# Kernel optimization log

Hardware: AMD Instinct MI355X
Metric: run time of the kernel (lower is better)

## Reference

```python
import jax, jax.numpy as jnp
import numpy as np

N = 100000
E = 3200000
F_IN = 128
HID = 16
C = 8


def setup_inputs() -> dict:
    key = jax.random.key(0)
    k1, k2, k3, k4 = jax.random.split(key, 4)
    x = jax.random.normal(k1, (N, F_IN), dtype=jnp.float32)
    edge_index = jax.random.randint(k2, (2, E), 0, N, dtype=jnp.int64)
    W1 = jax.random.normal(k3, (F_IN, HID), dtype=jnp.float32) * (1.0 / np.sqrt(F_IN))
    b1 = jnp.zeros((HID,), dtype=jnp.float32)
    W2 = jax.random.normal(k4, (HID, C), dtype=jnp.float32) * (1.0 / np.sqrt(HID))
    b2 = jnp.zeros((C,), dtype=jnp.float32)
    return {"x": x, "edge_index": edge_index, "W1": W1, "b1": b1, "W2": W2, "b2": b2, "num_nodes": N}


def gcn_conv(x, src, dst, norm, W, b, num_nodes):
    # x: [N, F_in], src/dst: [E+N] (self-loops appended), norm: [E+N]
    h = x @ W                                # dense transform first (small out dim)
    msg = h[src] * norm[:, None]             # gather + edgewise scale
    out = jax.ops.segment_sum(msg, dst, num_segments=num_nodes)  # scatter-add
    return out + b


def reference(x, edge_index, W1, b1, W2, b2, num_nodes):
    # GCN normalization with self-loops: D^-1/2 (A+I) D^-1/2
    loop = jnp.arange(num_nodes, dtype=edge_index.dtype)
    src = jnp.concatenate([edge_index[0], loop])
    dst = jnp.concatenate([edge_index[1], loop])
    deg = jax.ops.segment_sum(jnp.ones_like(dst, dtype=x.dtype), dst, num_segments=num_nodes)
    dinv = jnp.where(deg > 0, jax.lax.rsqrt(deg), 0.0)
    norm = dinv[src] * dinv[dst]             # [E+N]

    h = jax.nn.relu(gcn_conv(x, src, dst, norm, W1, b1, num_nodes))
    # Dropout(p=0.5) in eval mode -> identity
    logits = gcn_conv(h, src, dst, norm, W2, b2, num_nodes)
    return jax.nn.log_softmax(logits, axis=1)
```

## Files before the change

kernel.cpp:

```cpp
#include <hip/hip_runtime.h>
#include <hip/hip_fp16.h>
#include <math.h>

#define FIN 128
#define HID 16
#define NC 8
#define BSH 8
#define BUKN 256
#define MAXBUK 512
#define CAP 10240
#define EPT 8

__global__ void setup_kernel(const void* __restrict__ ei, int E, int N,
                             int* __restrict__ flag, int* __restrict__ pcur,
                             int nbuk) {
    int b = blockIdx.x * blockDim.x + threadIdx.x;
    if (b < nbuk) pcur[b * 16] = b * CAP;
    if (b == 0) {
        const long long* p = (const long long*)ei;
        int ok = 1;
        for (int i = 0; i < 16; ++i) {
            long long v = p[i];
            if (v < 0 || v >= (long long)N) { ok = 0; break; }
        }
        *flag = ok;
    }
}

__global__ __launch_bounds__(1024) void passA_kernel(
        const void* __restrict__ ei, int E, const int* __restrict__ flag,
        int* __restrict__ pcur, unsigned* __restrict__ pakbuf, int nbuk) {
    const int is64 = *flag;
    const int* __restrict__ e32 = (const int*)ei;
    const int vecOK = is64 ? ((E & 1) == 0) : ((E & 3) == 0);
    __shared__ int cnt[MAXBUK], sbase[MAXBUK];
    const int t = threadIdx.x;
    const int CH = 1024 * EPT;
    for (long long c0 = (long long)blockIdx.x * CH; c0 < E;
         c0 += (long long)gridDim.x * CH) {
        for (int i = t; i < nbuk; i += 1024) cnt[i] = 0;
        __syncthreads();
        const long long e0 = c0 + (long long)t * EPT;
        const bool full = vecOK && (e0 + EPT <= E);
        int bv[EPT], rk[EPT];
        unsigned pv[EPT];
        if (full) {
            int ds[EPT], ss[EPT];
            if (is64) {
                const int4* pd = (const int4*)(e32 + 2 * ((long long)E + e0));
                const int4* ps = (const int4*)(e32 + 2 * e0);
                int4 a = pd[0], b = pd[1], c = pd[2], d = pd[3];
                ds[0]=a.x; ds[1]=a.z; ds[2]=b.x; ds[3]=b.z;
                ds[4]=c.x; ds[5]=c.z; ds[6]=d.x; ds[7]=d.z;
                int4 e = ps[0], f = ps[1], g = ps[2], h = ps[3];
                ss[0]=e.x; ss[1]=e.z; ss[2]=f.x; ss[3]=f.z;
                ss[4]=g.x; ss[5]=g.z; ss[6]=h.x; ss[7]=h.z;
            } else {
                const int4* pd = (const int4*)(e32 + (long long)E + e0);
                const int4* ps = (const int4*)(e32 + e0);
                int4 a = pd[0], b = pd[1];
                ds[0]=a.x; ds[1]=a.y; ds[2]=a.z; ds[3]=a.w;
                ds[4]=b.x; ds[5]=b.y; ds[6]=b.z; ds[7]=b.w;
                int4 e = ps[0], f = ps[1];
                ss[0]=e.x; ss[1]=e.y; ss[2]=e.z; ss[3]=e.w;
                ss[4]=f.x; ss[5]=f.y; ss[6]=f.z; ss[7]=f.w;
            }
#pragma unroll
            for (int i = 0; i < EPT; ++i) {
                int dd = ds[i];
                bv[i] = dd >> BSH;
                pv[i] = (unsigned)ss[i] | ((unsigned)(dd & (BUKN - 1)) << 24);
                rk[i] = atomicAdd(&cnt[bv[i]], 1);
            }
        } else {
#pragma unroll
            for (int i = 0; i < EPT; ++i) {
                long long e = e0 + i;
                bv[i] = -1;
                if (e < E) {
                    int dd = e32[is64 ? 2 * ((long long)E + e) : ((long long)E + e)];
                    int ssc = e32[is64 ? 2 * e : e];
                    bv[i] = dd >> BSH;
                    pv[i] = (unsigned)ssc | ((unsigned)(dd & (BUKN - 1)) << 24);
                    rk[i] = atomicAdd(&cnt[bv[i]], 1);
                }
            }
        }
        __syncthreads();
        for (int i = t; i < nbuk; i += 1024)
            sbase[i] = cnt[i] ? atomicAdd(&pcur[i * 16], cnt[i]) : 0;
        __syncthreads();
#pragma unroll
        for (int i = 0; i < EPT; ++i) {
            if (bv[i] >= 0) {
                int pos = sbase[bv[i]] + rk[i];
                if (pos < (bv[i] + 1) * CAP) pakbuf[pos] = pv[i];
            }
        }
        __syncthreads();
    }
}

__global__ __launch_bounds__(512) void passC2_kernel(
        const unsigned* __restrict__ pak, const int* __restrict__ pcur,
        int* __restrict__ csr_src, int* __restrict__ off,
        float* __restrict__ dinv, int N) {
    __shared__ int c[BUKN], sc[BUKN], cur[BUKN];
    const int b = blockIdx.x, t = threadIdx.x;
    if (t < BUKN) c[t] = 0;
    __syncthreads();
    const int ebeg = b * CAP;
    int eend = pcur[b * 16];
    if (eend > ebeg + CAP) eend = ebeg + CAP;
    for (int i = ebeg + t; i < eend; i += 512)
        atomicAdd(&c[pak[i] >> 24], 1);
    __syncthreads();
    int v = (t < BUKN) ? c[t] : 0;
    if (t < BUKN) sc[t] = v;
    __syncthreads();
    for (int d = 1; d < 256; d <<= 1) {
        int add = (t < BUKN && t >= d) ? sc[t - d] : 0;
        __syncthreads();
        if (t < BUKN) sc[t] += add;
        __syncthreads();
    }
    if (t < BUKN) cur[t] = ebeg + sc[t] - v;
    __syncthreads();
    for (int i = ebeg + t; i < eend; i += 512) {
        unsigned w = pak[i];
        int pos = atomicAdd(&cur[w >> 24], 1);
        csr_src[pos] = (int)(w & 0xFFFFFFu);
    }
    __syncthreads();
    int n = (b << BSH) + t;
    if (t < BUKN && n < N) {
        off[n] = cur[t];
        dinv[n] = rsqrtf((float)(v + 1));
    }
}

__global__ void transform1_kernel(const float* __restrict__ x,
                                  const float* __restrict__ W1,
                                  const float* __restrict__ dinv,
                                  __half* __restrict__ g1, int N) {
    __shared__ float xs[16][FIN + 4];
    __shared__ float w[FIN][HID];
    const int t = threadIdx.x;
    for (int i = t; i < FIN * HID; i += 256) w[i / HID][i % HID] = W1[i];

    const float4* x4 = (const float4*)x;
    for (int rb = blockIdx.x * 16; rb < N; rb += gridDim.x * 16) {
        __syncthreads();
        for (int i = t; i < 16 * FIN / 4; i += 256) {
            int r = i >> 5, f4 = i & 31;
            int row = rb + r;
            float4 v = (row < N) ? x4[(size_t)row * (FIN / 4) + f4]
                                 : make_float4(0.f, 0.f, 0.f, 0.f);
            *((float4*)&xs[r][f4 * 4]) = v;
        }
        __syncthreads();
        int r = t >> 4, k = t & 15;
        int row = rb + r;
        if (row < N) {
            float s = 0.f;
#pragma unroll
            for (int f = 0; f < FIN; ++f) s += xs[r][f] * w[f][k];
            g1[(size_t)row * HID + k] = __float2half(s * dinv[row]);
        }
    }
}

__global__ void agg1_kernel(const int* __restrict__ off, const int* __restrict__ csr_src,
                            const __half2* __restrict__ g1h, const float* __restrict__ dinv,
                            const float* __restrict__ b1, float* __restrict__ h, int N) {
    const float4* g1q = (const float4*)g1h;
    int wid = threadIdx.x >> 6;
    int lane = threadIdx.x & 63;
    int sub = lane >> 4;
    int r = lane & 15;
    int hi = r & 1;
    int j = r >> 1;
    float4 bA = ((const float4*)b1)[hi * 2];
    float4 bB = ((const float4*)b1)[hi * 2 + 1];
    int wavesTotal = gridDim.x * (blockDim.x >> 6);
    for (int base = (blockIdx.x * (blockDim.x >> 6) + wid) * 4; base < N;
         base += wavesTotal * 4) {
        int n = base + sub;
        bool act = n < N;
        int start = 0, end = 0;
        float4 selfraw;
        if (act) {
            start = (n & (BUKN - 1)) ? off[n - 1] : (n >> BSH) * CAP;
            end = off[n];
            if (r < 2) selfraw = g1q[(size_t)n * 2 + hi];
        }
        float s0=0.f,s1=0.f,s2=0.f,s3=0.f,s4=0.f,s5=0.f,s6=0.f,s7=0.f;
        for (int e = start + j; e < end; e += 8) {
            float4 raw = g1q[(size_t)csr_src[e] * 2 + hi];
            float2 f0 = __half22float2(*(__half2*)&raw.x);
            float2 f1 = __half22float2(*(__half2*)&raw.y);
            float2 f2 = __half22float2(*(__half2*)&raw.z);
            float2 f3 = __half22float2(*(__half2*)&raw.w);
            s0 += f0.x; s1 += f0.y; s2 += f1.x; s3 += f1.y;
            s4 += f2.x; s5 += f2.y; s6 += f3.x; s7 += f3.y;
        }
#pragma unroll
        for (int m = 2; m <= 8; m <<= 1) {
            s0 += __shfl_xor(s0, m, 64); s1 += __shfl_xor(s1, m, 64);
            s2 += __shfl_xor(s2, m, 64); s3 += __shfl_xor(s3, m, 64);
            s4 += __shfl_xor(s4, m, 64); s5 += __shfl_xor(s5, m, 64);
            s6 += __shfl_xor(s6, m, 64); s7 += __shfl_xor(s7, m, 64);
        }
        if (act && r < 2) {
            float di = dinv[n];
            float2 f0 = __half22float2(*(__half2*)&selfraw.x);
            float2 f1 = __half22float2(*(__half2*)&selfraw.y);
            float2 f2 = __half22float2(*(__half2*)&selfraw.z);
            float2 f3 = __half22float2(*(__half2*)&selfraw.w);
            float4 oA, oB;
            oA.x = fmaxf(di * (s0 + f0.x) + bA.x, 0.f);
            oA.y = fmaxf(di * (s1 + f0.y) + bA.y, 0.f);
            oA.z = fmaxf(di * (s2 + f1.x) + bA.z, 0.f);
            oA.w = fmaxf(di * (s3 + f1.y) + bA.w, 0.f);
            oB.x = fmaxf(di * (s4 + f2.x) + bB.x, 0.f);
            oB.y = fmaxf(di * (s5 + f2.y) + bB.y, 0.f);
            oB.z = fmaxf(di * (s6 + f3.x) + bB.z, 0.f);
            oB.w = fmaxf(di * (s7 + f3.y) + bB.w, 0.f);
            float4* hp = (float4*)&h[(size_t)n * HID + hi * 8];
            hp[0] = oA; hp[1] = oB;
        }
    }
}

__global__ void transform2_kernel(const float* __restrict__ h,
                                  const float* __restrict__ W2,
                                  const float* __restrict__ dinv,
                                  __half* __restrict__ g2, int N) {
    int total = N * NC;
    for (int idx = blockIdx.x * blockDim.x + threadIdx.x; idx < total;
         idx += gridDim.x * blockDim.x) {
        int n = idx >> 3, c = idx & 7;
        float s = 0.f;
#pragma unroll
        for (int k = 0; k < HID; ++k) s += h[n * HID + k] * W2[k * NC + c];
        g2[idx] = __float2half(s * dinv[n]);
    }
}

__global__ void agg2_kernel(const int* __restrict__ off, const int* __restrict__ csr_src,
                            const __half2* __restrict__ g2h, const float* __restrict__ dinv,
                            const float* __restrict__ b2, float* __restrict__ out, int N) {
    const float4* g2q = (const float4*)g2h;
    int wid = threadIdx.x >> 6;
    int lane = threadIdx.x & 63;
    int sub = lane >> 3, sl = lane & 7;
    float4 b2A = ((const float4*)b2)[0];
    float4 b2B = ((const float4*)b2)[1];
    int wavesTotal = gridDim.x * (blockDim.x >> 6);
    for (int base = (blockIdx.x * (blockDim.x >> 6) + wid) * 8; base < N;
         base += wavesTotal * 8) {
        int n = base + sub;
        bool act = n < N;
        int start = 0, end = 0;
        float4 selfraw;
        if (act) {
            start = (n & (BUKN - 1)) ? off[n - 1] : (n >> BSH) * CAP;
            end = off[n];
            selfraw = g2q[n];
        }
        float s0=0.f,s1=0.f,s2=0.f,s3=0.f,s4=0.f,s5=0.f,s6=0.f,s7=0.f;
        for (int e = start + sl; e < end; e += 8) {
            float4 raw = g2q[csr_src[e]];
            float2 f0 = __half22float2(*(__half2*)&raw.x);
            float2 f1 = __half22float2(*(__half2*)&raw.y);
            float2 f2 = __half22float2(*(__half2*)&raw.z);
            float2 f3 = __half22float2(*(__half2*)&raw.w);
            s0 += f0.x; s1 += f0.y; s2 += f1.x; s3 += f1.y;
            s4 += f2.x; s5 += f2.y; s6 += f3.x; s7 += f3.y;
        }
#pragma unroll
        for (int m = 1; m <= 4; m <<= 1) {
            s0 += __shfl_xor(s0, m, 64); s1 += __shfl_xor(s1, m, 64);
            s2 += __shfl_xor(s2, m, 64); s3 += __shfl_xor(s3, m, 64);
            s4 += __shfl_xor(s4, m, 64); s5 += __shfl_xor(s5, m, 64);
            s6 += __shfl_xor(s6, m, 64); s7 += __shfl_xor(s7, m, 64);
        }
        if (act) {
            float di = dinv[n];
            float2 f0 = __half22float2(*(__half2*)&selfraw.x);
            float2 f1 = __half22float2(*(__half2*)&selfraw.y);
            float2 f2 = __half22float2(*(__half2*)&selfraw.z);
            float2 f3 = __half22float2(*(__half2*)&selfraw.w);
            float l0 = di * (s0 + f0.x) + b2A.x;
            float l1 = di * (s1 + f0.y) + b2A.y;
            float l2 = di * (s2 + f1.x) + b2A.z;
            float l3 = di * (s3 + f1.y) + b2A.w;
            float l4 = di * (s4 + f2.x) + b2B.x;
            float l5 = di * (s5 + f2.y) + b2B.y;
            float l6 = di * (s6 + f3.x) + b2B.z;
            float l7 = di * (s7 + f3.y) + b2B.w;
            float m0 = fmaxf(fmaxf(fmaxf(l0, l1), fmaxf(l2, l3)),
                             fmaxf(fmaxf(l4, l5), fmaxf(l6, l7)));
            float se = __expf(l0 - m0) + __expf(l1 - m0) + __expf(l2 - m0) +
                       __expf(l3 - m0) + __expf(l4 - m0) + __expf(l5 - m0) +
                       __expf(l6 - m0) + __expf(l7 - m0);
            float lse = m0 + __logf(se);
            if (sl < 2) {
                float4 o;
                if (sl == 0) { o.x=l0-lse; o.y=l1-lse; o.z=l2-lse; o.w=l3-lse; }
                else         { o.x=l4-lse; o.y=l5-lse; o.z=l6-lse; o.w=l7-lse; }
                ((float4*)&out[(size_t)n * NC])[sl] = o;
            }
        }
    }
}

extern "C" void kernel_launch(void* const* d_in, const int* in_sizes, int n_in,
                              void* d_out, int out_size, void* d_ws, size_t ws_size,
                              hipStream_t stream) {
    const float* x  = (const float*)d_in[0];
    const void*  ei = d_in[1];
    const float* W1 = (const float*)d_in[2];
    const float* b1 = (const float*)d_in[3];
    const float* W2 = (const float*)d_in[4];
    const float* b2 = (const float*)d_in[5];

    const int N = in_sizes[0] / FIN;
    const int E = in_sizes[1] / 2;
    const int nbuk = (N + BUKN - 1) >> BSH;

    char* p = (char*)d_ws;
    unsigned* pakbuf = (unsigned*)p;     p += (size_t)nbuk * CAP * 4;
    int*    csr_src = (int*)p;           p += (size_t)nbuk * CAP * 4;
    __half* g1h     = (__half*)p;        p += (size_t)N * HID * 2;
    float*  h       = (float*)p;         p += (size_t)N * HID * 4;
    __half* g2h     = (__half*)p;        p += (size_t)N * NC * 2;
    int*    off     = (int*)p;           p += (size_t)N * 4;
    float*  dinv    = (float*)p;         p += (size_t)N * 4;
    int*    pcur    = (int*)p;           p += (size_t)MAXBUK * 16 * 4;
    int*    flag    = (int*)p;

    setup_kernel<<<(nbuk + 255) / 256, 256, 0, stream>>>(ei, E, N, flag, pcur, nbuk);
    passA_kernel<<<(E + 8191) / 8192, 1024, 0, stream>>>(ei, E, flag, pcur,
                                                         pakbuf, nbuk);
    passC2_kernel<<<nbuk, 512, 0, stream>>>(pakbuf, pcur, csr_src, off, dinv, N);

    transform1_kernel<<<(N + 15) / 16, 256, 0, stream>>>(x, W1, dinv, g1h, N);
    agg1_kernel<<<(N + 15) / 16, 256, 0, stream>>>(off, csr_src, (const __half2*)g1h,
                                                   dinv, b1, h, N);
    transform2_kernel<<<2048, 256, 0, stream>>>(h, W2, dinv, g2h, N);
    agg2_kernel<<<(N + 31) / 32, 256, 0, stream>>>(off, csr_src, (const __half2*)g2h,
                                                   dinv, b2, (float*)d_out, N);
}
```

Baseline: 144.9 us.

## Fuse layer-2 transform into agg1 and stage bucket scatter through LDS

Folds the h@W2 transform and the dinv scaling into the agg1 epilogue: W2 is held in shared memory, each half-row computes a partial product, and the halves are combined with a lane shuffle before writing half-precision g2 directly. This removes the fp32 h buffer round trip and one kernel launch. Separately, passA now runs 512-thread blocks and block-sorts edges by bucket in LDS using a prefix scan. It then writes pakbuf contiguously per bucket to get more coalesced global stores, at the cost of extra syncs and scan work.

New measurement: 137.7 us. 1.05x faster.

```diff
diff --git a/kernel.cpp b/kernel.cpp
--- a/kernel.cpp
+++ b/kernel.cpp
@@ -10,6 +10,7 @@
 #define MAXBUK 512
 #define CAP 10240
 #define EPT 8
+#define ACH (512 * EPT)
 
 __global__ void setup_kernel(const void* __restrict__ ei, int E, int N,
                              int* __restrict__ flag, int* __restrict__ pcur,
@@ -27,18 +28,19 @@
     }
 }
 
-__global__ __launch_bounds__(1024) void passA_kernel(
+__global__ __launch_bounds__(512) void passA_kernel(
         const void* __restrict__ ei, int E, const int* __restrict__ flag,
         int* __restrict__ pcur, unsigned* __restrict__ pakbuf, int nbuk) {
     const int is64 = *flag;
     const int* __restrict__ e32 = (const int*)ei;
     const int vecOK = is64 ? ((E & 1) == 0) : ((E & 3) == 0);
-    __shared__ int cnt[MAXBUK], sbase[MAXBUK];
+    __shared__ int cnt[MAXBUK], scn[MAXBUK], sbase[MAXBUK];
+    __shared__ unsigned spv[ACH];
+    __shared__ unsigned short sbk[ACH];
     const int t = threadIdx.x;
-    const int CH = 1024 * EPT;
-    for (long long c0 = (long long)blockIdx.x * CH; c0 < E;
-         c0 += (long long)gridDim.x * CH) {
-        for (int i = t; i < nbuk; i += 1024) cnt[i] = 0;
+    for (long long c0 = (long long)blockIdx.x * ACH; c0 < E;
+         c0 += (long long)gridDim.x * ACH) {
+        cnt[t] = 0;
         __syncthreads();
         const long long e0 = c0 + (long long)t * EPT;
         const bool full = vecOK && (e0 + EPT <= E);
@@ -87,15 +89,34 @@
             }
         }
         __syncthreads();
-        for (int i = t; i < nbuk; i += 1024)
-            sbase[i] = cnt[i] ? atomicAdd(&pcur[i * 16], cnt[i]) : 0;
+        int v = cnt[t];
+        scn[t] = v;
+        __syncthreads();
+        for (int d = 1; d < MAXBUK; d <<= 1) {
+            int add = (t >= d) ? scn[t - d] : 0;
+            __syncthreads();
+            scn[t] += add;
+            __syncthreads();
+        }
+        int excl = scn[t] - v;
+        __syncthreads();
+        scn[t] = excl;
+        if (t < nbuk) sbase[t] = v ? atomicAdd(&pcur[t * 16], v) : 0;
         __syncthreads();
 #pragma unroll
         for (int i = 0; i < EPT; ++i) {
             if (bv[i] >= 0) {
-                int pos = sbase[bv[i]] + rk[i];
-                if (pos < (bv[i] + 1) * CAP) pakbuf[pos] = pv[i];
-            }
+                int s = scn[bv[i]] + rk[i];
+                spv[s] = pv[i];
+                sbk[s] = (unsigned short)bv[i];
+            }
+        }
+        __syncthreads();
+        int total = (int)((E - c0 < ACH) ? (E - c0) : ACH);
+        for (int s = t; s < total; s += 512) {
+            int b = sbk[s];
+            int gpos = sbase[b] + (s - scn[b]);
+            if (gpos < (b + 1) * CAP) pakbuf[gpos] = spv[s];
         }
         __syncthreads();
     }
@@ -172,8 +193,13 @@
 
 __global__ void agg1_kernel(const int* __restrict__ off, const int* __restrict__ csr_src,
                             const __half2* __restrict__ g1h, const float* __restrict__ dinv,
-                            const float* __restrict__ b1, float* __restrict__ h, int N) {
+                            const float* __restrict__ b1, const float* __restrict__ W2,
+                            float4* __restrict__ g2q_out, int N) {
     const float4* g1q = (const float4*)g1h;
+    __shared__ float w2s[HID][NC];
+    for (int i = threadIdx.x; i < HID * NC; i += blockDim.x)
+        w2s[i >> 3][i & 7] = W2[i];
+    __syncthreads();
     int wid = threadIdx.x >> 6;
     int lane = threadIdx.x & 63;
     int sub = lane >> 4;
@@ -217,33 +243,36 @@
             float2 f1 = __half22float2(*(__half2*)&selfraw.y);
             float2 f2 = __half22float2(*(__half2*)&selfraw.z);
             float2 f3 = __half22float2(*(__half2*)&selfraw.w);
-            float4 oA, oB;
-            oA.x = fmaxf(di * (s0 + f0.x) + bA.x, 0.f);
-            oA.y = fmaxf(di * (s1 + f0.y) + bA.y, 0.f);
-            oA.z = fmaxf(di * (s2 + f1.x) + bA.z, 0.f);
-            oA.w = fmaxf(di * (s3 + f1.y) + bA.w, 0.f);
-            oB.x = fmaxf(di * (s4 + f2.x) + bB.x, 0.f);
-            oB.y = fmaxf(di * (s5 + f2.y) + bB.y, 0.f);
-            oB.z = fmaxf(di * (s6 + f3.x) + bB.z, 0.f);
-            oB.w = fmaxf(di * (s7 + f3.y) + bB.w, 0.f);
-            float4* hp = (float4*)&h[(size_t)n * HID + hi * 8];
-            hp[0] = oA; hp[1] = oB;
-        }
-    }
-}
-
-__global__ void transform2_kernel(const float* __restrict__ h,
-                                  const float* __restrict__ W2,
-                                  const float* __restrict__ dinv,
-                                  __half* __restrict__ g2, int N) {
-    int total = N * NC;
-    for (int idx = blockIdx.x * blockDim.x + threadIdx.x; idx < total;
-         idx += gridDim.x * blockDim.x) {
-        int n = idx >> 3, c = idx & 7;
-        float s = 0.f;
-#pragma unroll
-        for (int k = 0; k < HID; ++k) s += h[n * HID + k] * W2[k * NC + c];
-        g2[idx] = __float2half(s * dinv[n]);
+            float h8[8];
+            h8[0] = fmaxf(di * (s0 + f0.x) + bA.x, 0.f);
+            h8[1] = fmaxf(di * (s1 + f0.y) + bA.y, 0.f);
+            h8[2] = fmaxf(di * (s2 + f1.x) + bA.z, 0.f);
+            h8[3] = fmaxf(di * (s3 + f1.y) + bA.w, 0.f);
+            h8[4] = fmaxf(di * (s4 + f2.x) + bB.x, 0.f);
+            h8[5] = fmaxf(di * (s5 + f2.y) + bB.y, 0.f);
+            h8[6] = fmaxf(di * (s6 + f3.x) + bB.z, 0.f);
+            h8[7] = fmaxf(di * (s7 + f3.y) + bB.w, 0.f);
+            float part[8];
+#pragma unroll
+            for (int c = 0; c < 8; ++c) {
+                float acc = 0.f;
+#pragma unroll
+                for (int k = 0; k < 8; ++k) acc += h8[k] * w2s[hi * 8 + k][c];
+                part[c] = acc;
+            }
+#pragma unroll
+            for (int c = 0; c < 8; ++c) part[c] += __shfl_xor(part[c], 1, 64);
+            if (r == 0) {
+                __half2 p0 = __floats2half2_rn(part[0] * di, part[1] * di);
+                __half2 p1 = __floats2half2_rn(part[2] * di, part[3] * di);
+                __half2 p2 = __floats2half2_rn(part[4] * di, part[5] * di);
+                __half2 p3 = __floats2half2_rn(part[6] * di, part[7] * di);
+                float4 o;
+                *(__half2*)&o.x = p0; *(__half2*)&o.y = p1;
+                *(__half2*)&o.z = p2; *(__half2*)&o.w = p3;
+                g2q_out[n] = o;
+            }
+        }
     }
 }
 
@@ -333,7 +362,6 @@
     unsigned* pakbuf = (unsigned*)p;     p += (size_t)nbuk * CAP * 4;
     int*    csr_src = (int*)p;           p += (size_t)nbuk * CAP * 4;
     __half* g1h     = (__half*)p;        p += (size_t)N * HID * 2;
-    float*  h       = (float*)p;         p += (size_t)N * HID * 4;
     __half* g2h     = (__half*)p;        p += (size_t)N * NC * 2;
     int*    off     = (int*)p;           p += (size_t)N * 4;
     float*  dinv    = (float*)p;         p += (size_t)N * 4;
@@ -341,14 +369,13 @@
     int*    flag    = (int*)p;
 
     setup_kernel<<<(nbuk + 255) / 256, 256, 0, stream>>>(ei, E, N, flag, pcur, nbuk);
-    passA_kernel<<<(E + 8191) / 8192, 1024, 0, stream>>>(ei, E, flag, pcur,
-                                                         pakbuf, nbuk);
+    passA_kernel<<<(E + ACH - 1) / ACH, 512, 0, stream>>>(ei, E, flag, pcur,
+                                                          pakbuf, nbuk);
     passC2_kernel<<<nbuk, 512, 0, stream>>>(pakbuf, pcur, csr_src, off, dinv, N);
 
     transform1_kernel<<<(N + 15) / 16, 256, 0, stream>>>(x, W1, dinv, g1h, N);
     agg1_kernel<<<(N + 15) / 16, 256, 0, stream>>>(off, csr_src, (const __half2*)g1h,
-                                                   dinv, b1, h, N);
-    transform2_kernel<<<2048, 256, 0, stream>>>(h, W2, dinv, g2h, N);
+                                                   dinv, b1, W2, (float4*)g2h, N);
     agg2_kernel<<<(N + 31) / 32, 256, 0, stream>>>(off, csr_src, (const __half2*)g2h,
                                                    dinv, b2, (float*)d_out, N);
 }
```
